# Performance work log

Hardware: AMD Instinct MI355X
Metric: run time of the kernel (lower is better)

Reference implementation:

```python
import jax, jax.numpy as jnp
import numpy as np

N = 50000        # nodes
E = 250000       # edges (avg degree 5)
D = 32           # embed_dim
N_LAYERS = 3


def _uniform(key, shape, fan_in):
    s = 1.0 / np.sqrt(fan_in)
    return jax.random.uniform(key, shape, jnp.float32, -s, s)


def setup_inputs() -> dict:
    key = jax.random.key(0)
    ks = jax.random.split(key, 10)
    x = jax.random.normal(ks[0], (N, 1), jnp.float32)
    edge_index = jax.random.randint(ks[1], (2, E), 0, N, dtype=jnp.int64)
    edge_attribute = jax.random.normal(ks[2], (E, 1), jnp.float32)
    # Linear weights stored as [in, out] (i.e. torch weight transposed)
    node_W = _uniform(ks[3], (1, D), 1)
    node_b = _uniform(ks[4], (D,), 1)
    l1_W = _uniform(ks[5], (1, D * D), 1)
    l1_b = _uniform(ks[6], (D * D,), 1)
    root = _uniform(ks[7], (D, D), D)      # NNConv root weight
    conv_b = _uniform(ks[8], (D,), D)      # NNConv bias
    return {
        "x": x, "edge_index": edge_index, "edge_attribute": edge_attribute,
        "i": 2, "dummy": 0,
        "node_W": node_W, "node_b": node_b,
        "l1_W": l1_W, "l1_b": l1_b,
        "root": root, "conv_b": conv_b,
    }


def reference(x, edge_index, edge_attribute, i, dummy, node_W, node_b,
              l1_W, l1_b, root, conv_b):
    n_encode_layers = min(i + 1, N_LAYERS)
    src, dst = edge_index[0], edge_index[1]

    # node embedding: [N,1] -> [N,D]
    h = x @ node_W + node_b

    # edge-conditioned weight matrices, shared by every layer: [E, D, D]
    We = (edge_attribute @ l1_W + l1_b).reshape(E, D, D)

    # mean-aggregation denominator (in-degree, clamped; isolated nodes -> 0 msg)
    cnt = jax.ops.segment_sum(jnp.ones((E,), h.dtype), dst, num_segments=N)
    cnt = jnp.maximum(cnt, 1.0)[:, None]

    for _ in range(n_encode_layers):
        h = jax.nn.relu(h)
        # gather source features, per-edge matmul: msg_e = x_src[e] @ We[e]
        msg = jnp.einsum('ei,eio->eo', h[src], We)
        aggr = jax.ops.segment_sum(msg, dst, num_segments=N) / cnt
        h = aggr + h @ root + conv_b
    return h
```

## Files before the change

kernel.cpp:

```cpp
#include <hip/hip_runtime.h>
#include <hip/hip_bf16.h>

#define N_NODES 50000
#define N_EDGES 250000
#define DIM 32
#define BLK 256
#define NTILES 196
#define PREP_NB 6250
#define WCONV_NB 25
#define LAYER_NB 3125

typedef __attribute__((ext_vector_type(8))) short short8;
typedef __attribute__((ext_vector_type(4))) float f32x4;

__device__ __forceinline__ float ldf(const void* p, int i, int isf32) {
    return isf32 ? ((const float*)p)[i]
                 : __bfloat162float(((const __hip_bfloat16*)p)[i]);
}
__device__ __forceinline__ int ldi(const int* ei, int i, int i64) {
    return i64 ? ei[2 * i] : ei[i];
}
__device__ __forceinline__ int clamp_idx(int v) {
    v = v < 0 ? 0 : v;
    return v >= N_NODES ? N_NODES - 1 : v;
}
__device__ __forceinline__ bool half_is_big(const void* p, int k) {
    unsigned short h = ((const unsigned short*)p)[k];
    float v = __uint_as_float(((unsigned int)h) << 16);
    return !(fabsf(v) <= 50.0f);
}
__device__ __forceinline__ unsigned short bf16bits(float v) {
    __hip_bfloat16 b = __float2bfloat16(v);
    return __builtin_bit_cast(unsigned short, b);
}

__global__ __launch_bounds__(BLK) void prep_kernel(
    const int* __restrict__ ei, const void* __restrict__ x,
    const void* __restrict__ nW, const void* __restrict__ nb,
    const void* __restrict__ lW, const void* __restrict__ lb,
    const void* __restrict__ rt, const void* __restrict__ cb,
    int* __restrict__ cntI, float* __restrict__ hrA, float* __restrict__ wsAll,
    unsigned short* __restrict__ wfrag)
{
    __shared__ int sdet;
    int tid = threadIdx.x;
    if (tid == 0) sdet = 0;
    __syncthreads();

    if (blockIdx.x >= PREP_NB) {
        if (tid < 64)       { if (half_is_big(lW, tid) || half_is_big(lW, tid + 64)) atomicOr(&sdet, 1); }
        else if (tid < 128) { int k = tid - 64;  if (half_is_big(lb, k) || half_is_big(lb, k + 64)) atomicOr(&sdet, 2); }
        else if (tid < 192) { int k = tid - 128; if (half_is_big(rt, k) || half_is_big(rt, k + 64)) atomicOr(&sdet, 4); }
        else if (tid < 224) { if (half_is_big(cb, tid - 192)) atomicOr(&sdet, 8); }
        __syncthreads();
        int fW = sdet & 1, fB = sdet & 2, fR = sdet & 4, fC = sdet & 8;
        int g = (int)(blockIdx.x - PREP_NB) * BLK + tid;
        if (g < 1024)       wsAll[g] = ldf(lW, g, fW);
        else if (g < 2048)  wsAll[g] = ldf(lb, g - 1024, fB);
        else if (g < 3072)  wsAll[g] = ldf(rt, g - 2048, fR);
        else if (g < 3104)  wsAll[g] = ldf(cb, g - 3072, fC);
        else if (g < 3104 + 3072) {
            int idx = g - 3104;
            int f = idx >> 9, rem = idx & 511;
            int ln = rem >> 3, j = rem & 7;
            int t = f >> 1, nh = f & 1;
            int k = t * 32 + (ln >> 4) * 8 + j;
            int n = nh * 16 + (ln & 15);
            float v;
            if (k < 32)      v = ldf(lW, k * 32 + n, fW);
            else if (k < 64) v = ldf(lb, (k - 32) * 32 + n, fB);
            else             v = ldf(rt, (k - 64) * 32 + n, fR);
            wfrag[idx] = bf16bits(v);
        }
        return;
    }

    if (tid < 64) {
        if (ei[2 * tid + 1] != 0) atomicOr(&sdet, 2);
    } else if (tid < 192) {
        int k = tid - 64;
        if (half_is_big(x, k)) atomicOr(&sdet, 4);
    } else {
        int k = tid - 192;
        if (k < 32) { if (half_is_big(nW, k)) atomicOr(&sdet, 8); }
        else        { if (half_is_big(nb, k - 32)) atomicOr(&sdet, 16); }
    }
    __syncthreads();
    int i64 = ((sdet & 2) == 0);
    int f_x = sdet & 4, f_nW = sdet & 8, f_nb = sdet & 16;

    int g = blockIdx.x * BLK + tid;
    if (g < N_EDGES) {
        int d = clamp_idx(ldi(ei, N_EDGES + g, i64));
        atomicAdd(&cntI[d], 1);
    }
    if (g < N_NODES * DIM) {
        int n = g >> 5, dd = g & 31;
        float hv = fmaf(ldf(x, n, f_x), ldf(nW, dd, f_nW), ldf(nb, dd, f_nb));
        hrA[g] = hv > 0.0f ? hv : 0.0f;
    }
}

__global__ __launch_bounds__(BLK) void scan_local_kernel(
    const int* __restrict__ cntI, int* __restrict__ rowstart, int* __restrict__ tsum)
{
    __shared__ int s0[BLK], s1[BLK];
    int t = threadIdx.x;
    int g = blockIdx.x * BLK + t;
    int v = (g < N_NODES) ? cntI[g] : 0;
    s0[t] = v;
    __syncthreads();
    int* s = s0; int* d = s1;
    for (int off = 1; off < BLK; off <<= 1) {
        int xv = s[t];
        if (t >= off) xv += s[t - off];
        d[t] = xv;
        __syncthreads();
        int* tmp = s; s = d; d = tmp;
    }
    int incl = s[t];
    if (g < N_NODES) rowstart[g] = incl - v;
    if (t == BLK - 1) tsum[blockIdx.x] = incl;
}

__global__ __launch_bounds__(BLK) void scatter_kernel(
    const int* __restrict__ ei, const void* __restrict__ ea,
    const int* __restrict__ rowstart, const int* __restrict__ tsum,
    int* __restrict__ edge_cur, int2* __restrict__ packed,
    int* __restrict__ rowG)
{
    __shared__ int sdet;
    __shared__ int stp[BLK], stx[BLK];
    int tid = threadIdx.x;
    if (tid == 0) sdet = 0;
    __syncthreads();
    if (tid < 64) {
        if (ei[2 * tid + 1] != 0) atomicOr(&sdet, 2);
    } else if (tid < 192) {
        int k = tid - 64;
        if (half_is_big(ea, k)) atomicOr(&sdet, 1);
    }
    int v = (tid < NTILES) ? tsum[tid] : 0;
    stp[tid] = v;
    __syncthreads();
    for (int off = 1; off < BLK; off <<= 1) {
        int xv = stp[tid];
        if (tid >= off) xv += stp[tid - off];
        __syncthreads();
        stp[tid] = xv;
        __syncthreads();
    }
    stx[tid] = stp[tid] - v;
    __syncthreads();
    int f_ea = sdet & 1, i64 = ((sdet & 2) == 0);

    int e = blockIdx.x * BLK + tid;
    if (e <= N_NODES)
        rowG[e] = (e == N_NODES) ? N_EDGES : rowstart[e] + stx[e >> 8];
    if (e < N_EDGES) {
        int s = clamp_idx(ldi(ei, e, i64));
        int d = clamp_idx(ldi(ei, N_EDGES + e, i64));
        float a = ldf(ea, e, f_ea);
        int slot = rowstart[d] + stx[d >> 8] + atomicAdd(&edge_cur[d], 1);
        packed[slot] = make_int2(s, __float_as_int(a));
    }
}

__global__ __launch_bounds__(BLK) void layer_kernel(
    const int2* __restrict__ packed, const int* __restrict__ rowG,
    const float* __restrict__ hin, const float* __restrict__ wsAll,
    const unsigned short* __restrict__ wfrag,
    float* __restrict__ outb, int last)
{
    __shared__ __align__(16) unsigned short sAu[16 * 96];
    int tid = threadIdx.x;
    int wv = tid >> 6;
    int lane = tid & 63;
    int half = lane >> 5;
    int l32 = lane & 31;
    int n0 = blockIdx.x * 16 + wv * 4;

    int S[5];
    #pragma unroll
    for (int j = 0; j < 5; ++j) S[j] = rowG[n0 + j];

    float hl01 = hin[n0 * DIM + lane];
    float hl23 = hin[(n0 + 2) * DIM + lane];

    int2 c[4][4];
    #pragma unroll
    for (int j = 0; j < 4; ++j) {
        #pragma unroll
        for (int i = 0; i < 4; ++i) {
            int k = S[j] + 2 * i + half;
            k = k < N_EDGES ? k : N_EDGES - 1;
            c[j][i] = packed[k];
        }
    }
    float h[4][4];
    #pragma unroll
    for (int j = 0; j < 4; ++j) {
        #pragma unroll
        for (int i = 0; i < 4; ++i)
            h[j][i] = hin[c[j][i].x * DIM + l32];
    }
    float p[4] = {0, 0, 0, 0}, q[4] = {0, 0, 0, 0};
    #pragma unroll
    for (int j = 0; j < 4; ++j) {
        #pragma unroll
        for (int i = 0; i < 4; ++i) {
            bool valid = (S[j] + 2 * i + half) < S[j + 1];
            float hv = valid ? h[j][i] : 0.0f;
            float a  = valid ? __int_as_float(c[j][i].y) : 0.0f;
            p[j] = fmaf(a, hv, p[j]);
            q[j] += hv;
        }
    }
    #pragma unroll
    for (int j = 0; j < 4; ++j) {
        for (int k = S[j] + 8 + half; k < S[j + 1]; k += 2) {
            int2 cc = packed[k];
            float hv = hin[cc.x * DIM + l32];
            p[j] = fmaf(__int_as_float(cc.y), hv, p[j]);
            q[j] += hv;
        }
    }
    #pragma unroll
    for (int j = 0; j < 4; ++j) {
        p[j] += __shfl_xor(p[j], 32);
        q[j] += __shfl_xor(q[j], 32);
        int dg = S[j + 1] - S[j];
        float ic = 1.0f / (dg < 1 ? 1.0f : (float)dg);
        p[j] *= ic;
        q[j] *= ic;
    }
    #pragma unroll
    for (int j = 0; j < 4; ++j)
        sAu[(wv * 4 + j) * 96 + half * 32 + l32] = bf16bits(half ? q[j] : p[j]);
    sAu[(wv * 4 + (lane >> 5)) * 96 + 64 + l32] = bf16bits(hl01);
    sAu[(wv * 4 + 2 + (lane >> 5)) * 96 + 64 + l32] = bf16bits(hl23);
    __syncthreads();

    if (wv < 2) {
        int nh = wv;
        short8 bfr[3];
        #pragma unroll
        for (int t = 0; t < 3; ++t)
            bfr[t] = *(const short8*)(wfrag + ((t * 2 + nh) * 64 + lane) * 8);
        f32x4 acc = {0.0f, 0.0f, 0.0f, 0.0f};
        #pragma unroll
        for (int t = 0; t < 3; ++t) {
            short8 afr = *(const short8*)(sAu + (lane & 15) * 96 + t * 32 + (lane >> 4) * 8);
            acc = __builtin_amdgcn_mfma_f32_16x16x32_bf16(afr, bfr[t], acc, 0, 0, 0);
        }
        float cbl = wsAll[3072 + nh * 16 + (lane & 15)];
        #pragma unroll
        for (int r = 0; r < 4; ++r) {
            int row = (lane >> 4) * 4 + r;
            float v = acc[r] + cbl;
            if (!last) v = v > 0.0f ? v : 0.0f;
            outb[(blockIdx.x * 16 + row) * DIM + nh * 16 + (lane & 15)] = v;
        }
    }
}

extern "C" void kernel_launch(void* const* d_in, const int* in_sizes, int n_in,
                              void* d_out, int out_size, void* d_ws, size_t ws_size,
                              hipStream_t stream) {
    const void* p[16];
    int np_ = 0;
    for (int i = 0; i < n_in && np_ < 16; ++i)
        if (in_sizes[i] != 1) p[np_++] = d_in[i];

    const void* x      = p[0];
    const int*  ei     = (const int*)p[1];
    const void* ea     = p[2];
    const void* node_W = p[3];
    const void* node_b = p[4];
    const void* l1_W   = p[5];
    const void* l1_b   = p[6];
    const void* root   = p[7];
    const void* conv_b = p[8];
    float* out = (float*)d_out;

    const int ND = N_NODES * DIM;
    float* ws = (float*)d_ws;
    int2*  packed   = (int2*)ws;
    float* hrA      = (float*)(packed + N_EDGES);
    float* hrB      = hrA + ND;
    float* wsAll    = hrB + ND;
    unsigned short* wfrag = (unsigned short*)(wsAll + 3104);
    int*   cntI     = (int*)(wfrag + 3072);
    int*   edge_cur = cntI + N_NODES;
    int*   rowstart = edge_cur + N_NODES;
    int*   tsum     = rowstart + N_NODES;
    int*   rowG     = tsum + 256;

    (void)hipMemsetAsync(cntI, 0, (size_t)(2 * N_NODES) * sizeof(int), stream);
    prep_kernel<<<PREP_NB + WCONV_NB, BLK, 0, stream>>>(
        ei, x, node_W, node_b, l1_W, l1_b, root, conv_b, cntI, hrA, wsAll, wfrag);
    scan_local_kernel<<<NTILES, BLK, 0, stream>>>(cntI, rowstart, tsum);
    scatter_kernel<<<(N_EDGES + BLK - 1) / BLK, BLK, 0, stream>>>(
        ei, ea, rowstart, tsum, edge_cur, packed, rowG);

    layer_kernel<<<LAYER_NB, BLK, 0, stream>>>(packed, rowG, hrA, wsAll, wfrag, hrB, 0);
    layer_kernel<<<LAYER_NB, BLK, 0, stream>>>(packed, rowG, hrB, wsAll, wfrag, hrA, 0);
    layer_kernel<<<LAYER_NB, BLK, 0, stream>>>(packed, rowG, hrA, wsAll, wfrag, out, 1);
}
```

Before: 165.0 us.

## Fuse degree histogram and local scan into prep, drop memset, widen layer blocks

```diff
diff --git a/kernel.cpp b/kernel.cpp
--- a/kernel.cpp
+++ b/kernel.cpp
@@ -4,11 +4,11 @@
 #define N_NODES 50000
 #define N_EDGES 250000
 #define DIM 32
-#define BLK 256
 #define NTILES 196
-#define PREP_NB 6250
-#define WCONV_NB 25
-#define LAYER_NB 3125
+#define HIST_NB NTILES
+#define HR_NB 6250
+#define WCONV_NB 13
+#define LAYER_NB 1563
 
 typedef __attribute__((ext_vector_type(8))) short short8;
 typedef __attribute__((ext_vector_type(4))) float f32x4;
@@ -34,103 +34,104 @@
     return __builtin_bit_cast(unsigned short, b);
 }
 
-__global__ __launch_bounds__(BLK) void prep_kernel(
+__global__ __launch_bounds__(256) void prep_kernel(
     const int* __restrict__ ei, const void* __restrict__ x,
     const void* __restrict__ nW, const void* __restrict__ nb,
     const void* __restrict__ lW, const void* __restrict__ lb,
     const void* __restrict__ rt, const void* __restrict__ cb,
-    int* __restrict__ cntI, float* __restrict__ hrA, float* __restrict__ wsAll,
-    unsigned short* __restrict__ wfrag)
+    int* __restrict__ rowstart, int* __restrict__ tsum,
+    int* __restrict__ edge_cur, float* __restrict__ hrA,
+    float* __restrict__ wCB, unsigned short* __restrict__ wfrag)
 {
     __shared__ int sdet;
     int tid = threadIdx.x;
+    int b = blockIdx.x;
     if (tid == 0) sdet = 0;
     __syncthreads();
 
-    if (blockIdx.x >= PREP_NB) {
-        if (tid < 64)       { if (half_is_big(lW, tid) || half_is_big(lW, tid + 64)) atomicOr(&sdet, 1); }
-        else if (tid < 128) { int k = tid - 64;  if (half_is_big(lb, k) || half_is_big(lb, k + 64)) atomicOr(&sdet, 2); }
-        else if (tid < 192) { int k = tid - 128; if (half_is_big(rt, k) || half_is_big(rt, k + 64)) atomicOr(&sdet, 4); }
-        else if (tid < 224) { if (half_is_big(cb, tid - 192)) atomicOr(&sdet, 8); }
-        __syncthreads();
-        int fW = sdet & 1, fB = sdet & 2, fR = sdet & 4, fC = sdet & 8;
-        int g = (int)(blockIdx.x - PREP_NB) * BLK + tid;
-        if (g < 1024)       wsAll[g] = ldf(lW, g, fW);
-        else if (g < 2048)  wsAll[g] = ldf(lb, g - 1024, fB);
-        else if (g < 3072)  wsAll[g] = ldf(rt, g - 2048, fR);
-        else if (g < 3104)  wsAll[g] = ldf(cb, g - 3072, fC);
-        else if (g < 3104 + 3072) {
-            int idx = g - 3104;
-            int f = idx >> 9, rem = idx & 511;
-            int ln = rem >> 3, j = rem & 7;
-            int t = f >> 1, nh = f & 1;
-            int k = t * 32 + (ln >> 4) * 8 + j;
-            int n = nh * 16 + (ln & 15);
-            float v;
-            if (k < 32)      v = ldf(lW, k * 32 + n, fW);
-            else if (k < 64) v = ldf(lb, (k - 32) * 32 + n, fB);
-            else             v = ldf(rt, (k - 64) * 32 + n, fR);
-            wfrag[idx] = bf16bits(v);
-        }
+    if (b < HIST_NB) {
+        __shared__ int hist[256], sscan[256];
+        hist[tid] = 0;
+        if (tid < 64) {
+            if (ei[2 * tid + 1] != 0) atomicOr(&sdet, 2);
+        }
+        __syncthreads();
+        int i64 = ((sdet & 2) == 0);
+        int tile = b;
+        for (int e = tid; e < N_EDGES; e += 256) {
+            int d = clamp_idx(ldi(ei, N_EDGES + e, i64));
+            if ((d >> 8) == tile) atomicAdd(&hist[d & 255], 1);
+        }
+        __syncthreads();
+        int v = hist[tid];
+        int* s = hist; int* d2 = sscan;
+        for (int off = 1; off < 256; off <<= 1) {
+            int xv = s[tid];
+            if (tid >= off) xv += s[tid - off];
+            d2[tid] = xv;
+            __syncthreads();
+            int* t = s; s = d2; d2 = t;
+        }
+        int incl = s[tid];
+        int g = tile * 256 + tid;
+        if (g < N_NODES) {
+            rowstart[g] = incl - v;
+            edge_cur[g] = 0;
+        }
+        if (tid == 255) tsum[tile] = incl;
         return;
     }
 
-    if (tid < 64) {
-        if (ei[2 * tid + 1] != 0) atomicOr(&sdet, 2);
-    } else if (tid < 192) {
-        int k = tid - 64;
-        if (half_is_big(x, k)) atomicOr(&sdet, 4);
-    } else {
-        int k = tid - 192;
-        if (k < 32) { if (half_is_big(nW, k)) atomicOr(&sdet, 8); }
-        else        { if (half_is_big(nb, k - 32)) atomicOr(&sdet, 16); }
-    }
-    __syncthreads();
-    int i64 = ((sdet & 2) == 0);
-    int f_x = sdet & 4, f_nW = sdet & 8, f_nb = sdet & 16;
-
-    int g = blockIdx.x * BLK + tid;
-    if (g < N_EDGES) {
-        int d = clamp_idx(ldi(ei, N_EDGES + g, i64));
-        atomicAdd(&cntI[d], 1);
-    }
-    if (g < N_NODES * DIM) {
-        int n = g >> 5, dd = g & 31;
-        float hv = fmaf(ldf(x, n, f_x), ldf(nW, dd, f_nW), ldf(nb, dd, f_nb));
-        hrA[g] = hv > 0.0f ? hv : 0.0f;
-    }
-}
-
-__global__ __launch_bounds__(BLK) void scan_local_kernel(
-    const int* __restrict__ cntI, int* __restrict__ rowstart, int* __restrict__ tsum)
-{
-    __shared__ int s0[BLK], s1[BLK];
-    int t = threadIdx.x;
-    int g = blockIdx.x * BLK + t;
-    int v = (g < N_NODES) ? cntI[g] : 0;
-    s0[t] = v;
-    __syncthreads();
-    int* s = s0; int* d = s1;
-    for (int off = 1; off < BLK; off <<= 1) {
-        int xv = s[t];
-        if (t >= off) xv += s[t - off];
-        d[t] = xv;
-        __syncthreads();
-        int* tmp = s; s = d; d = tmp;
-    }
-    int incl = s[t];
-    if (g < N_NODES) rowstart[g] = incl - v;
-    if (t == BLK - 1) tsum[blockIdx.x] = incl;
-}
-
-__global__ __launch_bounds__(BLK) void scatter_kernel(
+    if (b < HIST_NB + HR_NB) {
+        if (tid < 128) {
+            if (half_is_big(x, tid)) atomicOr(&sdet, 4);
+        } else if (tid < 160) {
+            if (half_is_big(nW, tid - 128)) atomicOr(&sdet, 8);
+        } else if (tid < 192) {
+            if (half_is_big(nb, tid - 160)) atomicOr(&sdet, 16);
+        }
+        __syncthreads();
+        int f_x = sdet & 4, f_nW = sdet & 8, f_nb = sdet & 16;
+        int g = (b - HIST_NB) * 256 + tid;
+        if (g < N_NODES * DIM) {
+            int n = g >> 5, dd = g & 31;
+            float hv = fmaf(ldf(x, n, f_x), ldf(nW, dd, f_nW), ldf(nb, dd, f_nb));
+            hrA[g] = hv > 0.0f ? hv : 0.0f;
+        }
+        return;
+    }
+
+    if (tid < 64)       { if (half_is_big(lW, tid) || half_is_big(lW, tid + 64)) atomicOr(&sdet, 1); }
+    else if (tid < 128) { int k = tid - 64;  if (half_is_big(lb, k) || half_is_big(lb, k + 64)) atomicOr(&sdet, 2); }
+    else if (tid < 192) { int k = tid - 128; if (half_is_big(rt, k) || half_is_big(rt, k + 64)) atomicOr(&sdet, 4); }
+    else if (tid < 224) { if (half_is_big(cb, tid - 192)) atomicOr(&sdet, 8); }
+    __syncthreads();
+    int fW = sdet & 1, fB = sdet & 2, fR = sdet & 4, fC = sdet & 8;
+    int g = (int)(b - HIST_NB - HR_NB) * 256 + tid;
+    if (g < 3072) {
+        int f = g >> 9, rem = g & 511;
+        int ln = rem >> 3, j = rem & 7;
+        int t = f >> 1, nh = f & 1;
+        int k = t * 32 + (ln >> 4) * 8 + j;
+        int n = nh * 16 + (ln & 15);
+        float v;
+        if (k < 32)      v = ldf(lW, k * 32 + n, fW);
+        else if (k < 64) v = ldf(lb, (k - 32) * 32 + n, fB);
+        else             v = ldf(rt, (k - 64) * 32 + n, fR);
+        wfrag[g] = bf16bits(v);
+    } else if (g < 3104) {
+        wCB[g - 3072] = ldf(cb, g - 3072, fC);
+    }
+}
+
+__global__ __launch_bounds__(256) void scatter_kernel(
     const int* __restrict__ ei, const void* __restrict__ ea,
     const int* __restrict__ rowstart, const int* __restrict__ tsum,
     int* __restrict__ edge_cur, int2* __restrict__ packed,
     int* __restrict__ rowG)
 {
     __shared__ int sdet;
-    __shared__ int stp[BLK], stx[BLK];
+    __shared__ int stp[256], stx[256];
     int tid = threadIdx.x;
     if (tid == 0) sdet = 0;
     __syncthreads();
@@ -143,7 +144,7 @@
     int v = (tid < NTILES) ? tsum[tid] : 0;
     stp[tid] = v;
     __syncthreads();
-    for (int off = 1; off < BLK; off <<= 1) {
+    for (int off = 1; off < 256; off <<= 1) {
         int xv = stp[tid];
         if (tid >= off) xv += stp[tid - off];
         __syncthreads();
@@ -154,7 +155,7 @@
     __syncthreads();
     int f_ea = sdet & 1, i64 = ((sdet & 2) == 0);
 
-    int e = blockIdx.x * BLK + tid;
+    int e = blockIdx.x * 256 + tid;
     if (e <= N_NODES)
         rowG[e] = (e == N_NODES) ? N_EDGES : rowstart[e] + stx[e >> 8];
     if (e < N_EDGES) {
@@ -166,23 +167,27 @@
     }
 }
 
-__global__ __launch_bounds__(BLK) void layer_kernel(
+__global__ __launch_bounds__(512) void layer_kernel(
     const int2* __restrict__ packed, const int* __restrict__ rowG,
-    const float* __restrict__ hin, const float* __restrict__ wsAll,
+    const float* __restrict__ hin, const float* __restrict__ wCB,
     const unsigned short* __restrict__ wfrag,
     float* __restrict__ outb, int last)
 {
-    __shared__ __align__(16) unsigned short sAu[16 * 96];
+    __shared__ __align__(16) unsigned short sAu[32 * 96];
     int tid = threadIdx.x;
     int wv = tid >> 6;
     int lane = tid & 63;
     int half = lane >> 5;
     int l32 = lane & 31;
-    int n0 = blockIdx.x * 16 + wv * 4;
+    int nbase = blockIdx.x * 32;
+    int n0 = nbase + wv * 4;
 
     int S[5];
     #pragma unroll
-    for (int j = 0; j < 5; ++j) S[j] = rowG[n0 + j];
+    for (int j = 0; j < 5; ++j) {
+        int n = n0 + j;
+        S[j] = rowG[n < N_NODES ? n : N_NODES];
+    }
 
     float hl01 = hin[n0 * DIM + lane];
     float hl23 = hin[(n0 + 2) * DIM + lane];
@@ -237,12 +242,12 @@
     #pragma unroll
     for (int j = 0; j < 4; ++j)
         sAu[(wv * 4 + j) * 96 + half * 32 + l32] = bf16bits(half ? q[j] : p[j]);
-    sAu[(wv * 4 + (lane >> 5)) * 96 + 64 + l32] = bf16bits(hl01);
-    sAu[(wv * 4 + 2 + (lane >> 5)) * 96 + 64 + l32] = bf16bits(hl23);
-    __syncthreads();
-
-    if (wv < 2) {
-        int nh = wv;
+    sAu[(wv * 4 + half) * 96 + 64 + l32] = bf16bits(hl01);
+    sAu[(wv * 4 + 2 + half) * 96 + 64 + l32] = bf16bits(hl23);
+    __syncthreads();
+
+    if (wv < 4) {
+        int rg = wv & 1, nh = wv >> 1;
         short8 bfr[3];
         #pragma unroll
         for (int t = 0; t < 3; ++t)
@@ -250,16 +255,20 @@
         f32x4 acc = {0.0f, 0.0f, 0.0f, 0.0f};
         #pragma unroll
         for (int t = 0; t < 3; ++t) {
-            short8 afr = *(const short8*)(sAu + (lane & 15) * 96 + t * 32 + (lane >> 4) * 8);
+            short8 afr = *(const short8*)(sAu + (rg * 16 + (lane & 15)) * 96
+                                          + t * 32 + (lane >> 4) * 8);
             acc = __builtin_amdgcn_mfma_f32_16x16x32_bf16(afr, bfr[t], acc, 0, 0, 0);
         }
-        float cbl = wsAll[3072 + nh * 16 + (lane & 15)];
+        float cbl = wCB[nh * 16 + (lane & 15)];
         #pragma unroll
         for (int r = 0; r < 4; ++r) {
-            int row = (lane >> 4) * 4 + r;
-            float v = acc[r] + cbl;
-            if (!last) v = v > 0.0f ? v : 0.0f;
-            outb[(blockIdx.x * 16 + row) * DIM + nh * 16 + (lane & 15)] = v;
+            int row = rg * 16 + (lane >> 4) * 4 + r;
+            int n = nbase + row;
+            if (n < N_NODES) {
+                float v = acc[r] + cbl;
+                if (!last) v = v > 0.0f ? v : 0.0f;
+                outb[n * DIM + nh * 16 + (lane & 15)] = v;
+            }
         }
     }
 }
@@ -288,22 +297,20 @@
     int2*  packed   = (int2*)ws;
     float* hrA      = (float*)(packed + N_EDGES);
     float* hrB      = hrA + ND;
-    float* wsAll    = hrB + ND;
-    unsigned short* wfrag = (unsigned short*)(wsAll + 3104);
-    int*   cntI     = (int*)(wfrag + 3072);
-    int*   edge_cur = cntI + N_NODES;
+    float* wCB      = hrB + ND;
+    unsigned short* wfrag = (unsigned short*)(wCB + 32);
+    int*   edge_cur = (int*)(wfrag + 3072);
     int*   rowstart = edge_cur + N_NODES;
     int*   tsum     = rowstart + N_NODES;
     int*   rowG     = tsum + 256;
 
-    (void)hipMemsetAsync(cntI, 0, (size_t)(2 * N_NODES) * sizeof(int), stream);
-    prep_kernel<<<PREP_NB + WCONV_NB, BLK, 0, stream>>>(
-        ei, x, node_W, node_b, l1_W, l1_b, root, conv_b, cntI, hrA, wsAll, wfrag);
-    scan_local_kernel<<<NTILES, BLK, 0, stream>>>(cntI, rowstart, tsum);
-    scatter_kernel<<<(N_EDGES + BLK - 1) / BLK, BLK, 0, stream>>>(
+    prep_kernel<<<HIST_NB + HR_NB + WCONV_NB, 256, 0, stream>>>(
+        ei, x, node_W, node_b, l1_W, l1_b, root, conv_b,
+        rowstart, tsum, edge_cur, hrA, wCB, wfrag);
+    scatter_kernel<<<(N_EDGES + 255) / 256, 256, 0, stream>>>(
         ei, ea, rowstart, tsum, edge_cur, packed, rowG);
 
-    layer_kernel<<<LAYER_NB, BLK, 0, stream>>>(packed, rowG, hrA, wsAll, wfrag, hrB, 0);
-    layer_kernel<<<LAYER_NB, BLK, 0, stream>>>(packed, rowG, hrB, wsAll, wfrag, hrA, 0);
-    layer_kernel<<<LAYER_NB, BLK, 0, stream>>>(packed, rowG, hrA, wsAll, wfrag, out, 1);
-}
+    layer_kernel<<<LAYER_NB, 512, 0, stream>>>(packed, rowG, hrA, wCB, wfrag, hrB, 0);
+    layer_kernel<<<LAYER_NB, 512, 0, stream>>>(packed, rowG, hrB, wCB, wfrag, hrA, 0);
+    layer_kernel<<<LAYER_NB, 512, 0, stream>>>(packed, rowG, hrA, wCB, wfrag, out, 1);
+}
```

New measurement: 421.4 us. +155.4%, slower.
